# Kernel optimization log

Measured on AMD Instinct MI355X. Metric: run time of the kernel, lower is better.

The kernel has to match this reference:

```python
import jax, jax.numpy as jnp
import numpy as np

B, N, F, I = 4, 1024, 32, 8
DIM, DN, NF = 256, 64, 100
H, HD = 4, 64  # heads, head_dim (H*HD == DIM)
EPS = 1e-5


def setup_inputs() -> dict:
    key = jax.random.key(0)
    ks = jax.random.split(key, 24)
    def p(k, shape, s=0.05):
        return jax.random.normal(k, shape, jnp.float32) * s
    return {
        "x": jax.random.normal(ks[0], (B, N, F, I), jnp.float32),
        "idx": jax.random.randint(ks[1], (F,), 0, NF),
        "ctx": jax.random.normal(ks[2], (B, 1, DN), jnp.float32),
        "Wp": p(ks[3], (NF, DIM * I)),          # in_projection table
        "Bp": p(ks[4], (NF, DIM)),               # feature_bias table
        "q_emb": p(ks[5], (1, DIM)),             # queries table
        "cln_kv_W": p(ks[6], (DN, 2 * DIM)), "cln_kv_b": jnp.zeros((2 * DIM,), jnp.float32),
        "cln_q_W": p(ks[7], (DN, 2 * DIM)),  "cln_q_b": jnp.zeros((2 * DIM,), jnp.float32),
        "cln_h_W": p(ks[8], (DN, 2 * DIM)),  "cln_h_b": jnp.zeros((2 * DIM,), jnp.float32),
        "Wq": p(ks[9], (DIM, DIM)), "Wk": p(ks[10], (DIM, DIM)),
        "Wv": p(ks[11], (DIM, DIM)), "Wo": p(ks[12], (DIM, DIM)),
        "W1": p(ks[13], (DIM, 4 * DIM)), "b1": jnp.zeros((4 * DIM,), jnp.float32),
        "W2": p(ks[14], (4 * DIM, DIM)), "b2": jnp.zeros((DIM,), jnp.float32),
    }


def _ln(x):
    m = x.mean(-1, keepdims=True)
    v = ((x - m) ** 2).mean(-1, keepdims=True)
    return (x - m) * jax.lax.rsqrt(v + EPS)


def _cln(x, c, W, b):
    # adaptive layernorm: ln(x) * (1 + scale(ctx)) + shift(ctx)
    h = _ln(x)
    s, sh = jnp.split(c @ W + b, 2, axis=-1)
    return h * (1.0 + s) + sh


def reference(x, idx, ctx, Wp, Bp, q_emb, cln_kv_W, cln_kv_b, cln_q_W, cln_q_b,
              cln_h_W, cln_h_b, Wq, Wk, Wv, Wo, W1, b1, W2, b2):
    b_, n_, f_, i_ = x.shape
    # gather per-feature projection weights and biases
    w = Wp[idx].reshape(f_, DIM, i_)                 # [f, d, i]
    bias = Bp[idx][None]                              # [1, f, d] (broadcasts b,n)
    kv = jnp.einsum('bnfi,fdi->bnfd', x, w)           # [b, n, f, d]
    c = ctx[:, :, None, :]                            # [b, 1, 1, dn]
    kv = _cln(kv, c, cln_kv_W, cln_kv_b) + bias
    q = jnp.broadcast_to(q_emb[None, None], (b_, n_, 1, DIM))
    # cross-attention (pre-norm, conditional)
    qn = _cln(q, c, cln_q_W, cln_q_b)
    qh = (qn @ Wq).reshape(b_, n_, 1, H, HD)
    kh = (kv @ Wk).reshape(b_, n_, f_, H, HD)
    vh = (kv @ Wv).reshape(b_, n_, f_, H, HD)
    att = jnp.einsum('bnqhe,bnfhe->bnhqf', qh, kh) / np.sqrt(HD).astype(np.float32)
    att = jax.nn.softmax(att, axis=-1)
    o = jnp.einsum('bnhqf,bnfhe->bnqhe', att, vh).reshape(b_, n_, 1, DIM) @ Wo
    h = q + o
    # MLP (pre-norm, conditional)
    hn = _cln(h, c, cln_h_W, cln_h_b)
    h = h + (jax.nn.gelu(hn @ W1 + b1) @ W2 + b2)
    return h[:, :, 0, :]                              # squeeze query dim -> [b, n, d]
```

## Files before the change

kernel.cpp:

```cpp
#include <hip/hip_runtime.h>
#include <cmath>

#define EPSV 1e-5f
using f4 = float4;

typedef __attribute__((ext_vector_type(8))) short bfrag;
typedef __attribute__((ext_vector_type(4))) float ffrag;

#define WS_SKV   0
#define WS_SHKV  1024
#define WS_SH    2048
#define WS_SHH   3072
#define WS_A     4096
#define WS_R     8192
#define WS_HT    4202496
#define WS_L     5251072
#define WS_G     6299648
#define WS_GB    WS_G
#define WS_HNB   (WS_G + 2097152)
#define WS_W1T   (WS_G + 2621440)
#define WS_W2T   (WS_G + 2752512)
#define WS_MT    (WS_G + 2883584)

#define FMA8(acc, s, wa, wb) \
  acc[0]=fmaf((s),(wa).x,acc[0]); acc[1]=fmaf((s),(wa).y,acc[1]); \
  acc[2]=fmaf((s),(wa).z,acc[2]); acc[3]=fmaf((s),(wa).w,acc[3]); \
  acc[4]=fmaf((s),(wb).x,acc[4]); acc[5]=fmaf((s),(wb).y,acc[5]); \
  acc[6]=fmaf((s),(wb).z,acc[6]); acc[7]=fmaf((s),(wb).w,acc[7]);

#define DOT8(res, v, wa, wb) \
  res = fmaf((v)[0],(wa).x,res); res = fmaf((v)[1],(wa).y,res); \
  res = fmaf((v)[2],(wa).z,res); res = fmaf((v)[3],(wa).w,res); \
  res = fmaf((v)[4],(wb).x,res); res = fmaf((v)[5],(wb).y,res); \
  res = fmaf((v)[6],(wb).z,res); res = fmaf((v)[7],(wb).w,res);

__device__ __forceinline__ float bfly32(float v){
  v += __shfl_xor(v, 1);  v += __shfl_xor(v, 2);  v += __shfl_xor(v, 4);
  v += __shfl_xor(v, 8);  v += __shfl_xor(v, 16);
  return v;
}

template<int CTRL>
__device__ __forceinline__ float dpp_add(float v){
  int x = __builtin_bit_cast(int, v);
  int y = __builtin_amdgcn_update_dpp(0, x, CTRL, 0xf, 0xf, true);
  return v + __builtin_bit_cast(float, y);
}
__device__ __forceinline__ float red32(float v){
  v = dpp_add<0xB1>(v);
  v = dpp_add<0x4E>(v);
  v = dpp_add<0x124>(v);
  v = dpp_add<0x128>(v);
  v += __shfl_xor(v, 16);
  return v;
}

__device__ __forceinline__ float gelu_fast(float x){
  float z2 = 1.5957691216057308f*(x + 0.044715f*x*x*x);
  return x / (1.0f + __expf(-z2));
}

__device__ __forceinline__ unsigned short f2bf(float x){
  union { float f; unsigned u; } v; v.f = x;
  unsigned r = v.u + 0x7fffu + ((v.u >> 16) & 1u);
  return (unsigned short)(r >> 16);
}
__device__ __forceinline__ float bfu(unsigned short u){
  union { unsigned u; float f; } v; v.u = ((unsigned)u) << 16; return v.f;
}
__device__ __forceinline__ ushort4 comb4(ushort4 a, ushort4 b, float inv){
  ushort4 r;
  r.x = f2bf((bfu(a.x)+bfu(b.x))*inv);
  r.y = f2bf((bfu(a.y)+bfu(b.y))*inv);
  r.z = f2bf((bfu(a.z)+bfu(b.z))*inv);
  r.w = f2bf((bfu(a.w)+bfu(b.w))*inv);
  return r;
}

__global__ __launch_bounds__(256) void kwm_conv(
  const float* __restrict__ W1, const float* __restrict__ W2,
  const float* __restrict__ Wv, const float* __restrict__ Wo,
  float* __restrict__ ws)
{
  const int tid = threadIdx.x;
  int blk = blockIdx.x;
  if (blk < 128){
    __shared__ unsigned short lt[64][68];
    const float* src; unsigned short* dst; int K, N, K0, N0;
    if (blk < 64){
      src = W1; dst = (unsigned short*)(ws + WS_W1T);
      K = 256; N = 1024; K0 = (blk >> 4)*64; N0 = (blk & 15)*64;
    } else {
      blk -= 64;
      src = W2; dst = (unsigned short*)(ws + WS_W2T);
      K = 1024; N = 256; K0 = (blk >> 2)*64; N0 = (blk & 3)*64;
    }
    #pragma unroll
    for (int i=0;i<4;++i){
      int r = i*16 + (tid>>4);
      int c = (tid&15)*4;
      f4 v = *(const f4*)(src + (size_t)(K0+r)*N + N0 + c);
      lt[r][c]   = f2bf(v.x); lt[r][c+1] = f2bf(v.y);
      lt[r][c+2] = f2bf(v.z); lt[r][c+3] = f2bf(v.w);
    }
    __syncthreads();
    #pragma unroll
    for (int i=0;i<4;++i){
      int n  = i*16 + (tid>>4);
      int kc = (tid&15)*4;
      ushort4 u;
      u.x = lt[kc][n]; u.y = lt[kc+1][n]; u.z = lt[kc+2][n]; u.w = lt[kc+3][n];
      *(ushort4*)(dst + (size_t)(N0+n)*K + K0 + kc) = u;
    }
  } else {
    blk -= 128;
    __shared__ float wvs[4*64];
    __shared__ float wos[64*256];
    const int h   = blk >> 6;
    const int dg4 = blk & 63;
    {
      int d = tid >> 6, e = tid & 63;
      wvs[d*64+e] = Wv[(size_t)(dg4*4 + d)*256 + h*64 + e];
    }
    {
      int e = tid >> 2, c = (tid & 3)*64;
      const float* src = Wo + (size_t)(h*64 + e)*256 + c;
      #pragma unroll
      for (int i=0;i<16;++i)
        *(f4*)&wos[e*256 + c + i*4] = *(const f4*)(src + i*4);
    }
    __syncthreads();
    float acc[4] = {};
    for (int e=0;e<64;++e){
      float wo = wos[e*256 + tid];
      acc[0] = fmaf(wvs[0*64+e], wo, acc[0]);
      acc[1] = fmaf(wvs[1*64+e], wo, acc[1]);
      acc[2] = fmaf(wvs[2*64+e], wo, acc[2]);
      acc[3] = fmaf(wvs[3*64+e], wo, acc[3]);
    }
    unsigned short* Mt = (unsigned short*)(ws + WS_MT);
    ushort4 u;
    u.x = f2bf(acc[0]); u.y = f2bf(acc[1]); u.z = f2bf(acc[2]); u.w = f2bf(acc[3]);
    *(ushort4*)(Mt + (size_t)tid*1024 + h*256 + dg4*4) = u;
  }
}

__global__ __launch_bounds__(256) void k0_all(
    const float* __restrict__ ctx, const float* __restrict__ q_emb,
    const float* __restrict__ Wkv, const float* __restrict__ bkv,
    const float* __restrict__ Wqc, const float* __restrict__ bqc,
    const float* __restrict__ Whc, const float* __restrict__ bhc,
    const float* __restrict__ Wq,  const float* __restrict__ Wk,
    float* __restrict__ ws)
{
  const int b = blockIdx.x >> 2, h = blockIdx.x & 3;
  const int tid = threadIdx.x;
  __shared__ float c[64], qn[256], ph[256], qh64[64], red[8];
  if (tid < 64) c[tid] = ctx[b*64 + tid];
  __syncthreads();

  float skv = bkv[tid],      shkv = bkv[256+tid];
  float sq  = bqc[tid],      shq  = bqc[256+tid];
  float sh  = bhc[tid],      shh  = bhc[256+tid];
  #pragma unroll 8
  for (int j=0;j<64;++j){
    float cj = c[j];
    skv  = fmaf(cj, Wkv[j*512 + tid],       skv);
    shkv = fmaf(cj, Wkv[j*512 + 256 + tid], shkv);
    sq   = fmaf(cj, Wqc[j*512 + tid],       sq);
    shq  = fmaf(cj, Wqc[j*512 + 256 + tid], shq);
    sh   = fmaf(cj, Whc[j*512 + tid],       sh);
    shh  = fmaf(cj, Whc[j*512 + 256 + tid], shh);
  }
  if (h == 0){
    ws[WS_SKV  + b*256 + tid] = skv;
    ws[WS_SHKV + b*256 + tid] = shkv;
    ws[WS_SH   + b*256 + tid] = sh;
    ws[WS_SHH  + b*256 + tid] = shh;
  }

  float qe = q_emb[tid];
  float s1r = qe, s2r = qe*qe;
  for (int mm=1;mm<64;mm<<=1){ s1r += __shfl_xor(s1r,mm); s2r += __shfl_xor(s2r,mm); }
  int wv = tid>>6, ln = tid&63;
  if (ln==0){ red[wv*2]=s1r; red[wv*2+1]=s2r; }
  __syncthreads();
  float S1 = red[0]+red[2]+red[4]+red[6];
  float S2 = red[1]+red[3]+red[5]+red[7];
  float mean = S1*(1.0f/256.0f);
  float var  = S2*(1.0f/256.0f) - mean*mean;
  float rs   = rsqrtf(var + EPSV);
  qn[tid] = (qe-mean)*rs*(1.0f+sq) + shq;
  __syncthreads();

  {
    const int t = tid & 63, ks = tid >> 6;
    float p = 0.f;
    const float* wq = Wq + (size_t)(ks*64)*256 + h*64 + t;
    #pragma unroll 8
    for (int d=0; d<64; ++d) p = fmaf(qn[ks*64+d], wq[d*256], p);
    ph[tid] = p;
  }
  __syncthreads();
  if (tid < 64) qh64[tid] = ph[tid] + ph[64+tid] + ph[128+tid] + ph[192+tid];
  __syncthreads();

  {
    float a = 0.f;
    const float* wkr = Wk + (size_t)tid*256 + h*64;
    #pragma unroll
    for (int e4=0; e4<16; ++e4){
      f4 wv4 = *(const f4*)(wkr + e4*4);
      a = fmaf(qh64[e4*4+0], wv4.x, a);
      a = fmaf(qh64[e4*4+1], wv4.y, a);
      a = fmaf(qh64[e4*4+2], wv4.z, a);
      a = fmaf(qh64[e4*4+3], wv4.w, a);
    }
    ws[WS_A + b*1024 + h*256 + tid] = 0.125f*a;
  }
}

__global__ __launch_bounds__(256,4) void k1f_attn(
  const float* __restrict__ x, const int* __restrict__ idx,
  const float* __restrict__ Wp, const float* __restrict__ Bp,
  float* __restrict__ ws)
{
  __shared__ float xs[2048];
  __shared__ float wls[4096];

  const int tid = threadIdx.x;
  const int p0  = (blockIdx.x >> 1) * 8;
  const int half= blockIdx.x & 1;
  const int f0  = half * 16;
  const int b   = p0 >> 10;
  const int t   = tid >> 5;
  const int dg  = tid & 31;
  const int dA  = 4*dg, dB = 128 + 4*dg;

  {
    const float* xg = x + (size_t)p0*256 + tid*8;
    f4 a  = *(const f4*)xg;
    f4 bq = *(const f4*)(xg + 4);
    *(f4*)&xs[tid*8]     = a;
    *(f4*)&xs[tid*8 + 4] = bq;
  }
  f4 Ar[4][2];
  #pragma unroll
  for (int h=0;h<4;++h){
    Ar[h][0] = *(const f4*)(ws + WS_A + b*1024 + h*256 + dA);
    Ar[h][1] = *(const f4*)(ws + WS_A + b*1024 + h*256 + dB);
  }

  f4 skA = *(const f4*)(ws + WS_SKV  + b*256 + dA);
  f4 skB = *(const f4*)(ws + WS_SKV  + b*256 + dB);
  f4 shA = *(const f4*)(ws + WS_SHKV + b*256 + dA);
  f4 shB = *(const f4*)(ws + WS_SHKV + b*256 + dB);
  float coef[8] = {1.f+skA.x,1.f+skA.y,1.f+skA.z,1.f+skA.w,
                   1.f+skB.x,1.f+skB.y,1.f+skB.z,1.f+skB.w};
  float shk[8]  = {shA.x,shA.y,shA.z,shA.w, shB.x,shB.y,shB.z,shB.w};

  int r0 = idx[f0], r1 = idx[f0+1];
  f4 u0 = *(const f4*)(Wp + (size_t)r0*2048 + tid*8);
  f4 u1 = *(const f4*)(Wp + (size_t)r0*2048 + tid*8 + 4);
  f4 u2 = *(const f4*)(Wp + (size_t)r1*2048 + tid*8);
  f4 u3 = *(const f4*)(Wp + (size_t)r1*2048 + tid*8 + 4);

  float l[4] = {0.f,0.f,0.f,0.f};
  float racc[4][8] = {};

  for (int fi = 0; fi < 8; ++fi){
    const int f = f0 + fi*2;
    __syncthreads();
    wls[0*256+tid]=u0.x; wls[1*256+tid]=u0.y; wls[2*256+tid]=u0.z; wls[3*256+tid]=u0.w;
    wls[4*256+tid]=u1.x; wls[5*256+tid]=u1.y; wls[6*256+tid]=u1.z; wls[7*256+tid]=u1.w;
    wls[2048+0*256+tid]=u2.x; wls[2048+1*256+tid]=u2.y;
    wls[2048+2*256+tid]=u2.z; wls[2048+3*256+tid]=u2.w;
    wls[2048+4*256+tid]=u3.x; wls[2048+5*256+tid]=u3.y;
    wls[2048+6*256+tid]=u3.z; wls[2048+7*256+tid]=u3.w;
    __syncthreads();

    f4 ba0 = *(const f4*)(Bp + (size_t)r0*256 + dA);
    f4 bb0 = *(const f4*)(Bp + (size_t)r0*256 + dB);
    f4 ba1 = *(const f4*)(Bp + (size_t)r1*256 + dA);
    f4 bb1 = *(const f4*)(Bp + (size_t)r1*256 + dB);

    const int fn = (fi < 7) ? f + 2 : f0;
    int rn0 = idx[fn], rn1 = idx[fn+1];
    u0 = *(const f4*)(Wp + (size_t)rn0*2048 + tid*8);
    u1 = *(const f4*)(Wp + (size_t)rn0*2048 + tid*8 + 4);
    u2 = *(const f4*)(Wp + (size_t)rn1*2048 + tid*8);
    u3 = *(const f4*)(Wp + (size_t)rn1*2048 + tid*8 + 4);

    #pragma unroll
    for (int sub=0; sub<2; ++sub){
      const float* wrow = wls + sub*2048;
      const int fc = f + sub;
      f4 ba = sub ? ba1 : ba0;
      f4 bb = sub ? bb1 : bb0;

      f4 xa = *(const f4*)&xs[t*256 + fc*8];
      f4 xb = *(const f4*)&xs[t*256 + fc*8 + 4];
      float xf[8] = {xa.x,xa.y,xa.z,xa.w, xb.x,xb.y,xb.z,xb.w};

      float val[8] = {};
      #pragma unroll
      for (int i=0;i<8;++i){
        f4 wa  = *(const f4*)&wrow[i*256 + dA];
        f4 wbv = *(const f4*)&wrow[i*256 + dB];
        FMA8(val, xf[i], wa, wbv);
      }

      float s=0.f, ss=0.f;
      #pragma unroll
      for (int jj=0;jj<8;++jj){ s += val[jj]; ss = fmaf(val[jj],val[jj],ss); }
      s = red32(s); ss = red32(ss);
      float mean = s*(1.f/256.f);
      float var  = ss*(1.f/256.f) - mean*mean;
      float rsg  = rsqrtf(var + EPSV);
      float mrs  = mean*rsg;

      float off[8] = {shk[0]+ba.x, shk[1]+ba.y, shk[2]+ba.z, shk[3]+ba.w,
                      shk[4]+bb.x, shk[5]+bb.y, shk[6]+bb.z, shk[7]+bb.w};
      float kvl[8];
      #pragma unroll
      for (int jj=0;jj<8;++jj)
        kvl[jj] = fmaf(fmaf(val[jj], rsg, -mrs), coef[jj], off[jj]);

      #pragma unroll
      for (int h=0;h<4;++h){
        float lg = 0.f;
        DOT8(lg, kvl, Ar[h][0], Ar[h][1]);
        lg = red32(lg);
        float pp = __expf(lg);
        l[h] += pp;
        #pragma unroll
        for (int jj=0;jj<8;++jj)
          racc[h][jj] = fmaf(pp, kvl[jj], racc[h][jj]);
      }
    }
    r0 = rn0; r1 = rn1;
  }

  unsigned short* Pr = (unsigned short*)(ws + WS_R);
  size_t base = (size_t)(half*4096 + p0 + t) * 1024;
  #pragma unroll
  for (int h=0;h<4;++h){
    ushort4 ua, ub;
    ua.x=f2bf(racc[h][0]); ua.y=f2bf(racc[h][1]); ua.z=f2bf(racc[h][2]); ua.w=f2bf(racc[h][3]);
    ub.x=f2bf(racc[h][4]); ub.y=f2bf(racc[h][5]); ub.z=f2bf(racc[h][6]); ub.w=f2bf(racc[h][7]);
    *(ushort4*)(Pr + base + h*256 + dA) = ua;
    *(ushort4*)(Pr + base + h*256 + dB) = ub;
  }
  if (dg == 0){
    float* Lp = ws + WS_L;
    #pragma unroll
    for (int h=0;h<4;++h) Lp[(size_t)(half*4096 + p0 + t)*4 + h] = l[h];
  }
}

__global__ __launch_bounds__(256) void k2g_mfma(float* __restrict__ ws)
{
  __shared__ unsigned short aT[2][32*40];
  __shared__ unsigned short bT[2][64*40];
  __shared__ float invs[128];
  const unsigned short* P0 = (const unsigned short*)(ws + WS_R);
  const unsigned short* P1 = P0 + 4194304;
  const unsigned short* mt = (const unsigned short*)(ws + WS_MT);
  const float* Lp = ws + WS_L;

  const int tid = threadIdx.x;
  const int M0 = (blockIdx.x >> 2) * 32;
  const int N0 = (blockIdx.x & 3) * 64;
  const int lane = tid & 63;
  const int wid = tid >> 6;
  const int wm = wid >> 1, wn = wid & 1;
  const int m16 = lane & 15, q = lane >> 4;

  const int sa_m = tid >> 3, sa_k = (tid & 7) * 4;
  const int sb_n = tid >> 2, sb_k = (tid & 3) * 8;

  if (tid < 128){
    int lt = tid >> 2, h = tid & 3;
    invs[tid] = 1.f / (Lp[(size_t)(M0 + lt)*4 + h] +
                       Lp[(size_t)(4096 + M0 + lt)*4 + h]);
  }

  ushort4 ua0 = *(const ushort4*)(P0 + (size_t)(M0 + sa_m)*1024 + sa_k);
  ushort4 ua1 = *(const ushort4*)(P1 + (size_t)(M0 + sa_m)*1024 + sa_k);
  f4 ub = *(const f4*)(mt + (size_t)(N0 + sb_n)*1024 + sb_k);
  __syncthreads();

  ffrag acc[2];
  acc[0] = (ffrag){0.f,0.f,0.f,0.f};
  acc[1] = (ffrag){0.f,0.f,0.f,0.f};

  for (int ks=0; ks<32; ++ks){
    const int buf = ks & 1;
    float inv = invs[sa_m*4 + (ks >> 3)];
    *(ushort4*)&aT[buf][sa_m*40 + sa_k] = comb4(ua0, ua1, inv);
    *(f4*)&bT[buf][sb_n*40 + sb_k]      = ub;
    __syncthreads();
    int kn = (ks < 31) ? ks+1 : 31;
    ua0 = *(const ushort4*)(P0 + (size_t)(M0 + sa_m)*1024 + kn*32 + sa_k);
    ua1 = *(const ushort4*)(P1 + (size_t)(M0 + sa_m)*1024 + kn*32 + sa_k);
    ub  = *(const f4*)(mt + (size_t)(N0 + sb_n)*1024 + kn*32 + sb_k);

    bfrag af, bf0, bf1;
    af  = *(const bfrag*)&aT[buf][(wm*16 + m16)*40 + q*8];
    bf0 = *(const bfrag*)&bT[buf][(wn*32 + m16)*40 + q*8];
    bf1 = *(const bfrag*)&bT[buf][(wn*32 + 16 + m16)*40 + q*8];
    acc[0] = __builtin_amdgcn_mfma_f32_16x16x32_bf16(bf0, af, acc[0], 0, 0, 0);
    acc[1] = __builtin_amdgcn_mfma_f32_16x16x32_bf16(bf1, af, acc[1], 0, 0, 0);
  }

  const int m = M0 + wm*16 + m16;
  #pragma unroll
  for (int j=0;j<2;++j){
    const int n4 = N0 + wn*32 + j*16 + q*4;
    *(f4*)(ws + WS_HT + (size_t)m*256 + n4) =
      make_float4(acc[j][0], acc[j][1], acc[j][2], acc[j][3]);
  }
}

__global__ __launch_bounds__(256) void ke_ln(
  const float* __restrict__ q_emb, float* __restrict__ ws)
{
  const int tid = threadIdx.x;
  const int p0 = blockIdx.x * 8;
  const int b  = p0 >> 10;
  const int tq = tid >> 5, jq = tid & 31;
  const int cA = 4*jq, cB = 128 + 4*jq;

  float* op = ws + WS_HT + (size_t)(p0+tq)*256;
  f4 oA = *(const f4*)(op + cA);
  f4 oB = *(const f4*)(op + cB);
  f4 qA = *(const f4*)(q_emb + cA);
  f4 qB = *(const f4*)(q_emb + cB);
  float ht[8] = {oA.x+qA.x, oA.y+qA.y, oA.z+qA.z, oA.w+qA.w,
                 oB.x+qB.x, oB.y+qB.y, oB.z+qB.z, oB.w+qB.w};
  float s=0.f, ss=0.f;
  #pragma unroll
  for (int jj=0;jj<8;++jj){ s += ht[jj]; ss = fmaf(ht[jj],ht[jj],ss); }
  s = bfly32(s); ss = bfly32(ss);
  float mean = s*(1.f/256.f);
  float var  = ss*(1.f/256.f) - mean*mean;
  float rsg  = rsqrtf(var + EPSV);
  f4 sH0 = *(const f4*)(ws + WS_SH  + b*256 + cA);
  f4 sH1 = *(const f4*)(ws + WS_SH  + b*256 + cB);
  f4 hH0 = *(const f4*)(ws + WS_SHH + b*256 + cA);
  f4 hH1 = *(const f4*)(ws + WS_SHH + b*256 + cB);
  float sHv[8]  = {sH0.x,sH0.y,sH0.z,sH0.w, sH1.x,sH1.y,sH1.z,sH1.w};
  float hHv[8]  = {hH0.x,hH0.y,hH0.z,hH0.w, hH1.x,hH1.y,hH1.z,hH1.w};
  float hnv[8];
  #pragma unroll
  for (int jj=0;jj<8;++jj)
    hnv[jj] = (ht[jj]-mean)*rsg*(1.f+sHv[jj]) + hHv[jj];

  *(f4*)(op+cA) = make_float4(ht[0],ht[1],ht[2],ht[3]);
  *(f4*)(op+cB) = make_float4(ht[4],ht[5],ht[6],ht[7]);
  unsigned short* hnb = (unsigned short*)(ws + WS_HNB);
  ushort4 uA, uB;
  uA.x=f2bf(hnv[0]); uA.y=f2bf(hnv[1]); uA.z=f2bf(hnv[2]); uA.w=f2bf(hnv[3]);
  uB.x=f2bf(hnv[4]); uB.y=f2bf(hnv[5]); uB.z=f2bf(hnv[6]); uB.w=f2bf(hnv[7]);
  *(ushort4*)(hnb + (size_t)(p0+tq)*256 + cA) = uA;
  *(ushort4*)(hnb + (size_t)(p0+tq)*256 + cB) = uB;
}

__global__ __launch_bounds__(256) void k3_mfma(
  const float* __restrict__ b1, float* __restrict__ ws)
{
  __shared__ unsigned short aT[2][64*40];
  __shared__ unsigned short bT[2][128*40];
  const unsigned short* hnb = (const unsigned short*)(ws + WS_HNB);
  const unsigned short* w1t = (const unsigned short*)(ws + WS_W1T);
  unsigned short* gb = (unsigned short*)(ws + WS_GB);

  const int tid = threadIdx.x;
  const int M0 = (blockIdx.x >> 3) * 64;
  const int N0 = (blockIdx.x & 7) * 128;
  const int lane = tid & 63;
  const int wid = tid >> 6;
  const int wm = wid >> 1, wn = wid & 1;
  const int m16 = lane & 15, q = lane >> 4;

  const int sa_m = tid >> 2, sa_k = (tid & 3) * 8;
  const int sb_n = tid >> 1, sb_k = (tid & 1) * 16;

  f4 ua, ub0, ub1;
  ua  = *(const f4*)(hnb + (size_t)(M0 + sa_m)*256 + sa_k);
  ub0 = *(const f4*)(w1t + (size_t)(N0 + sb_n)*256 + sb_k);
  ub1 = *(const f4*)(w1t + (size_t)(N0 + sb_n)*256 + sb_k + 8);

  ffrag acc[2][4];
  #pragma unroll
  for (int i=0;i<2;++i)
    #pragma unroll
    for (int j=0;j<4;++j) acc[i][j] = (ffrag){0.f,0.f,0.f,0.f};

  for (int ks=0; ks<8; ++ks){
    const int buf = ks & 1;
    *(f4*)&aT[buf][sa_m*40 + sa_k]     = ua;
    *(f4*)&bT[buf][sb_n*40 + sb_k]     = ub0;
    *(f4*)&bT[buf][sb_n*40 + sb_k + 8] = ub1;
    __syncthreads();
    int kn = (ks < 7) ? ks+1 : 7;
    ua  = *(const f4*)(hnb + (size_t)(M0 + sa_m)*256 + kn*32 + sa_k);
    ub0 = *(const f4*)(w1t + (size_t)(N0 + sb_n)*256 + kn*32 + sb_k);
    ub1 = *(const f4*)(w1t + (size_t)(N0 + sb_n)*256 + kn*32 + sb_k + 8);

    bfrag af[2], bf_[4];
    af[0] = *(const bfrag*)&aT[buf][(wm*32 + m16)*40 + q*8];
    af[1] = *(const bfrag*)&aT[buf][(wm*32 + 16 + m16)*40 + q*8];
    #pragma unroll
    for (int j=0;j<4;++j)
      bf_[j] = *(const bfrag*)&bT[buf][(wn*64 + j*16 + m16)*40 + q*8];
    #pragma unroll
    for (int i=0;i<2;++i)
      #pragma unroll
      for (int j=0;j<4;++j)
        acc[i][j] = __builtin_amdgcn_mfma_f32_16x16x32_bf16(bf_[j], af[i], acc[i][j], 0, 0, 0);
  }

  #pragma unroll
  for (int i=0;i<2;++i){
    const int m = M0 + wm*32 + i*16 + m16;
    #pragma unroll
    for (int j=0;j<4;++j){
      const int n4 = N0 + wn*64 + j*16 + q*4;
      f4 bv = *(const f4*)(b1 + n4);
      ushort4 u;
      u.x = f2bf(gelu_fast(acc[i][j][0] + bv.x));
      u.y = f2bf(gelu_fast(acc[i][j][1] + bv.y));
      u.z = f2bf(gelu_fast(acc[i][j][2] + bv.z));
      u.w = f2bf(gelu_fast(acc[i][j][3] + bv.w));
      *(ushort4*)(gb + (size_t)m*1024 + n4) = u;
    }
  }
}

__global__ __launch_bounds__(256) void k4_mfma(
  const float* __restrict__ b2, const float* __restrict__ ws_c,
  float* __restrict__ ws, float* __restrict__ out)
{
  __shared__ unsigned short aT[2][32*40];
  __shared__ unsigned short bT[2][64*40];
  const unsigned short* gb  = (const unsigned short*)(ws_c + WS_GB);
  const unsigned short* w2t = (const unsigned short*)(ws_c + WS_W2T);

  const int tid = threadIdx.x;
  const int M0 = (blockIdx.x >> 2) * 32;
  const int N0 = (blockIdx.x & 3) * 64;
  const int lane = tid & 63;
  const int wid = tid >> 6;
  const int wm = wid >> 1, wn = wid & 1;
  const int m16 = lane & 15, q = lane >> 4;

  const int sa_m = tid >> 3, sa_k = (tid & 7) * 4;
  const int sb_n = tid >> 2, sb_k = (tid & 3) * 8;

  ushort4 ua;
  f4 ub;
  ua = *(const ushort4*)(gb  + (size_t)(M0 + sa_m)*1024 + sa_k);
  ub = *(const f4*)(w2t + (size_t)(N0 + sb_n)*1024 + sb_k);

  ffrag acc[2];
  acc[0] = (ffrag){0.f,0.f,0.f,0.f};
  acc[1] = (ffrag){0.f,0.f,0.f,0.f};

  for (int ks=0; ks<32; ++ks){
    const int buf = ks & 1;
    *(ushort4*)&aT[buf][sa_m*40 + sa_k] = ua;
    *(f4*)&bT[buf][sb_n*40 + sb_k]      = ub;
    __syncthreads();
    int kn = (ks < 31) ? ks+1 : 31;
    ua = *(const ushort4*)(gb  + (size_t)(M0 + sa_m)*1024 + kn*32 + sa_k);
    ub = *(const f4*)(w2t + (size_t)(N0 + sb_n)*1024 + kn*32 + sb_k);

    bfrag af, bf0, bf1;
    af  = *(const bfrag*)&aT[buf][(wm*16 + m16)*40 + q*8];
    bf0 = *(const bfrag*)&bT[buf][(wn*32 + m16)*40 + q*8];
    bf1 = *(const bfrag*)&bT[buf][(wn*32 + 16 + m16)*40 + q*8];
    acc[0] = __builtin_amdgcn_mfma_f32_16x16x32_bf16(bf0, af, acc[0], 0, 0, 0);
    acc[1] = __builtin_amdgcn_mfma_f32_16x16x32_bf16(bf1, af, acc[1], 0, 0, 0);
  }

  const int m = M0 + wm*16 + m16;
  #pragma unroll
  for (int j=0;j<2;++j){
    const int n4 = N0 + wn*32 + j*16 + q*4;
    f4 bv = *(const f4*)(b2 + n4);
    f4 hv = *(const f4*)(ws + WS_HT + (size_t)m*256 + n4);
    *(f4*)(out + (size_t)m*256 + n4) =
      make_float4(acc[j][0]+bv.x+hv.x, acc[j][1]+bv.y+hv.y,
                  acc[j][2]+bv.z+hv.z, acc[j][3]+bv.w+hv.w);
  }
}

extern "C" void kernel_launch(void* const* d_in, const int* in_sizes, int n_in,
                              void* d_out, int out_size, void* d_ws, size_t ws_size,
                              hipStream_t stream)
{
  const float* x    = (const float*)d_in[0];
  const int*   idx  = (const int*)  d_in[1];
  const float* ctx  = (const float*)d_in[2];
  const float* Wp   = (const float*)d_in[3];
  const float* Bp   = (const float*)d_in[4];
  const float* qemb = (const float*)d_in[5];
  const float* Wkv  = (const float*)d_in[6];
  const float* bkv  = (const float*)d_in[7];
  const float* Wqc  = (const float*)d_in[8];
  const float* bqc  = (const float*)d_in[9];
  const float* Whc  = (const float*)d_in[10];
  const float* bhc  = (const float*)d_in[11];
  const float* Wq   = (const float*)d_in[12];
  const float* Wk   = (const float*)d_in[13];
  const float* Wv   = (const float*)d_in[14];
  const float* Wo   = (const float*)d_in[15];
  const float* W1   = (const float*)d_in[16];
  const float* b1   = (const float*)d_in[17];
  const float* W2   = (const float*)d_in[18];
  const float* b2   = (const float*)d_in[19];
  float* ws  = (float*)d_ws;
  float* out = (float*)d_out;

  hipLaunchKernelGGL(kwm_conv, dim3(384),  dim3(256), 0, stream, W1, W2, Wv, Wo, ws);
  hipLaunchKernelGGL(k0_all,   dim3(16),   dim3(256), 0, stream,
                     ctx, qemb, Wkv, bkv, Wqc, bqc, Whc, bhc, Wq, Wk, ws);
  hipLaunchKernelGGL(k1f_attn, dim3(1024), dim3(256), 0, stream, x, idx, Wp, Bp, ws);
  hipLaunchKernelGGL(k2g_mfma, dim3(512),  dim3(256), 0, stream, ws);
  hipLaunchKernelGGL(ke_ln,    dim3(512),  dim3(256), 0, stream, qemb, ws);
  hipLaunchKernelGGL(k3_mfma,  dim3(512),  dim3(256), 0, stream, b1, ws);
  hipLaunchKernelGGL(k4_mfma,  dim3(512),  dim3(256), 0, stream, b2, ws, ws, out);
}
```

Before: 193.8 us.

## Merge prep kernels, process two tokens per attention thread, fuse output GEMM with LN

```diff
diff --git a/kernel.cpp b/kernel.cpp
--- a/kernel.cpp
+++ b/kernel.cpp
@@ -77,15 +77,25 @@
   return r;
 }
 
-__global__ __launch_bounds__(256) void kwm_conv(
+__global__ __launch_bounds__(256) void kprep(
   const float* __restrict__ W1, const float* __restrict__ W2,
   const float* __restrict__ Wv, const float* __restrict__ Wo,
+  const float* __restrict__ ctx, const float* __restrict__ q_emb,
+  const float* __restrict__ Wkv, const float* __restrict__ bkv,
+  const float* __restrict__ Wqc, const float* __restrict__ bqc,
+  const float* __restrict__ Whc, const float* __restrict__ bhc,
+  const float* __restrict__ Wq,  const float* __restrict__ Wk,
   float* __restrict__ ws)
 {
   const int tid = threadIdx.x;
   int blk = blockIdx.x;
+  __shared__ union {
+    unsigned short lt[64][68];
+    struct { float wvs[4*64]; float wos[64*256]; } m;
+    struct { float c[64], qn[256], ph[256], qh64[64], red[8]; } z;
+  } sm;
+
   if (blk < 128){
-    __shared__ unsigned short lt[64][68];
     const float* src; unsigned short* dst; int K, N, K0, N0;
     if (blk < 64){
       src = W1; dst = (unsigned short*)(ws + WS_W1T);
@@ -100,8 +110,8 @@
       int r = i*16 + (tid>>4);
       int c = (tid&15)*4;
       f4 v = *(const f4*)(src + (size_t)(K0+r)*N + N0 + c);
-      lt[r][c]   = f2bf(v.x); lt[r][c+1] = f2bf(v.y);
-      lt[r][c+2] = f2bf(v.z); lt[r][c+3] = f2bf(v.w);
+      sm.lt[r][c]   = f2bf(v.x); sm.lt[r][c+1] = f2bf(v.y);
+      sm.lt[r][c+2] = f2bf(v.z); sm.lt[r][c+3] = f2bf(v.w);
     }
     __syncthreads();
     #pragma unroll
@@ -109,127 +119,115 @@
       int n  = i*16 + (tid>>4);
       int kc = (tid&15)*4;
       ushort4 u;
-      u.x = lt[kc][n]; u.y = lt[kc+1][n]; u.z = lt[kc+2][n]; u.w = lt[kc+3][n];
+      u.x = sm.lt[kc][n]; u.y = sm.lt[kc+1][n]; u.z = sm.lt[kc+2][n]; u.w = sm.lt[kc+3][n];
       *(ushort4*)(dst + (size_t)(N0+n)*K + K0 + kc) = u;
     }
-  } else {
+  } else if (blk < 384){
     blk -= 128;
-    __shared__ float wvs[4*64];
-    __shared__ float wos[64*256];
     const int h   = blk >> 6;
     const int dg4 = blk & 63;
     {
       int d = tid >> 6, e = tid & 63;
-      wvs[d*64+e] = Wv[(size_t)(dg4*4 + d)*256 + h*64 + e];
+      sm.m.wvs[d*64+e] = Wv[(size_t)(dg4*4 + d)*256 + h*64 + e];
     }
     {
       int e = tid >> 2, c = (tid & 3)*64;
       const float* src = Wo + (size_t)(h*64 + e)*256 + c;
       #pragma unroll
       for (int i=0;i<16;++i)
-        *(f4*)&wos[e*256 + c + i*4] = *(const f4*)(src + i*4);
+        *(f4*)&sm.m.wos[e*256 + c + i*4] = *(const f4*)(src + i*4);
     }
     __syncthreads();
     float acc[4] = {};
     for (int e=0;e<64;++e){
-      float wo = wos[e*256 + tid];
-      acc[0] = fmaf(wvs[0*64+e], wo, acc[0]);
-      acc[1] = fmaf(wvs[1*64+e], wo, acc[1]);
-      acc[2] = fmaf(wvs[2*64+e], wo, acc[2]);
-      acc[3] = fmaf(wvs[3*64+e], wo, acc[3]);
+      float wo = sm.m.wos[e*256 + tid];
+      acc[0] = fmaf(sm.m.wvs[0*64+e], wo, acc[0]);
+      acc[1] = fmaf(sm.m.wvs[1*64+e], wo, acc[1]);
+      acc[2] = fmaf(sm.m.wvs[2*64+e], wo, acc[2]);
+      acc[3] = fmaf(sm.m.wvs[3*64+e], wo, acc[3]);
     }
     unsigned short* Mt = (unsigned short*)(ws + WS_MT);
     ushort4 u;
     u.x = f2bf(acc[0]); u.y = f2bf(acc[1]); u.z = f2bf(acc[2]); u.w = f2bf(acc[3]);
     *(ushort4*)(Mt + (size_t)tid*1024 + h*256 + dg4*4) = u;
-  }
-}
-
-__global__ __launch_bounds__(256) void k0_all(
-    const float* __restrict__ ctx, const float* __restrict__ q_emb,
-    const float* __restrict__ Wkv, const float* __restrict__ bkv,
-    const float* __restrict__ Wqc, const float* __restrict__ bqc,
-    const float* __restrict__ Whc, const float* __restrict__ bhc,
-    const float* __restrict__ Wq,  const float* __restrict__ Wk,
-    float* __restrict__ ws)
-{
-  const int b = blockIdx.x >> 2, h = blockIdx.x & 3;
-  const int tid = threadIdx.x;
-  __shared__ float c[64], qn[256], ph[256], qh64[64], red[8];
-  if (tid < 64) c[tid] = ctx[b*64 + tid];
-  __syncthreads();
-
-  float skv = bkv[tid],      shkv = bkv[256+tid];
-  float sq  = bqc[tid],      shq  = bqc[256+tid];
-  float sh  = bhc[tid],      shh  = bhc[256+tid];
-  #pragma unroll 8
-  for (int j=0;j<64;++j){
-    float cj = c[j];
-    skv  = fmaf(cj, Wkv[j*512 + tid],       skv);
-    shkv = fmaf(cj, Wkv[j*512 + 256 + tid], shkv);
-    sq   = fmaf(cj, Wqc[j*512 + tid],       sq);
-    shq  = fmaf(cj, Wqc[j*512 + 256 + tid], shq);
-    sh   = fmaf(cj, Whc[j*512 + tid],       sh);
-    shh  = fmaf(cj, Whc[j*512 + 256 + tid], shh);
-  }
-  if (h == 0){
-    ws[WS_SKV  + b*256 + tid] = skv;
-    ws[WS_SHKV + b*256 + tid] = shkv;
-    ws[WS_SH   + b*256 + tid] = sh;
-    ws[WS_SHH  + b*256 + tid] = shh;
-  }
-
-  float qe = q_emb[tid];
-  float s1r = qe, s2r = qe*qe;
-  for (int mm=1;mm<64;mm<<=1){ s1r += __shfl_xor(s1r,mm); s2r += __shfl_xor(s2r,mm); }
-  int wv = tid>>6, ln = tid&63;
-  if (ln==0){ red[wv*2]=s1r; red[wv*2+1]=s2r; }
-  __syncthreads();
-  float S1 = red[0]+red[2]+red[4]+red[6];
-  float S2 = red[1]+red[3]+red[5]+red[7];
-  float mean = S1*(1.0f/256.0f);
-  float var  = S2*(1.0f/256.0f) - mean*mean;
-  float rs   = rsqrtf(var + EPSV);
-  qn[tid] = (qe-mean)*rs*(1.0f+sq) + shq;
-  __syncthreads();
-
-  {
-    const int t = tid & 63, ks = tid >> 6;
-    float p = 0.f;
-    const float* wq = Wq + (size_t)(ks*64)*256 + h*64 + t;
+  } else {
+    blk -= 384;
+    const int b = blk >> 2, h = blk & 3;
+    if (tid < 64) sm.z.c[tid] = ctx[b*64 + tid];
+    __syncthreads();
+
+    float skv = bkv[tid],      shkv = bkv[256+tid];
+    float sq  = bqc[tid],      shq  = bqc[256+tid];
+    float sh  = bhc[tid],      shh  = bhc[256+tid];
     #pragma unroll 8
-    for (int d=0; d<64; ++d) p = fmaf(qn[ks*64+d], wq[d*256], p);
-    ph[tid] = p;
-  }
-  __syncthreads();
-  if (tid < 64) qh64[tid] = ph[tid] + ph[64+tid] + ph[128+tid] + ph[192+tid];
-  __syncthreads();
-
-  {
-    float a = 0.f;
-    const float* wkr = Wk + (size_t)tid*256 + h*64;
-    #pragma unroll
-    for (int e4=0; e4<16; ++e4){
-      f4 wv4 = *(const f4*)(wkr + e4*4);
-      a = fmaf(qh64[e4*4+0], wv4.x, a);
-      a = fmaf(qh64[e4*4+1], wv4.y, a);
-      a = fmaf(qh64[e4*4+2], wv4.z, a);
-      a = fmaf(qh64[e4*4+3], wv4.w, a);
-    }
-    ws[WS_A + b*1024 + h*256 + tid] = 0.125f*a;
-  }
-}
-
-__global__ __launch_bounds__(256,4) void k1f_attn(
+    for (int j=0;j<64;++j){
+      float cj = sm.z.c[j];
+      skv  = fmaf(cj, Wkv[j*512 + tid],       skv);
+      shkv = fmaf(cj, Wkv[j*512 + 256 + tid], shkv);
+      sq   = fmaf(cj, Wqc[j*512 + tid],       sq);
+      shq  = fmaf(cj, Wqc[j*512 + 256 + tid], shq);
+      sh   = fmaf(cj, Whc[j*512 + tid],       sh);
+      shh  = fmaf(cj, Whc[j*512 + 256 + tid], shh);
+    }
+    if (h == 0){
+      ws[WS_SKV  + b*256 + tid] = skv;
+      ws[WS_SHKV + b*256 + tid] = shkv;
+      ws[WS_SH   + b*256 + tid] = sh;
+      ws[WS_SHH  + b*256 + tid] = shh;
+    }
+
+    float qe = q_emb[tid];
+    float s1r = qe, s2r = qe*qe;
+    for (int mm=1;mm<64;mm<<=1){ s1r += __shfl_xor(s1r,mm); s2r += __shfl_xor(s2r,mm); }
+    int wv = tid>>6, ln = tid&63;
+    if (ln==0){ sm.z.red[wv*2]=s1r; sm.z.red[wv*2+1]=s2r; }
+    __syncthreads();
+    float S1 = sm.z.red[0]+sm.z.red[2]+sm.z.red[4]+sm.z.red[6];
+    float S2 = sm.z.red[1]+sm.z.red[3]+sm.z.red[5]+sm.z.red[7];
+    float mean = S1*(1.0f/256.0f);
+    float var  = S2*(1.0f/256.0f) - mean*mean;
+    float rs   = rsqrtf(var + EPSV);
+    sm.z.qn[tid] = (qe-mean)*rs*(1.0f+sq) + shq;
+    __syncthreads();
+
+    {
+      const int t = tid & 63, ks = tid >> 6;
+      float p = 0.f;
+      const float* wq = Wq + (size_t)(ks*64)*256 + h*64 + t;
+      #pragma unroll 8
+      for (int d=0; d<64; ++d) p = fmaf(sm.z.qn[ks*64+d], wq[d*256], p);
+      sm.z.ph[tid] = p;
+    }
+    __syncthreads();
+    if (tid < 64) sm.z.qh64[tid] = sm.z.ph[tid] + sm.z.ph[64+tid] + sm.z.ph[128+tid] + sm.z.ph[192+tid];
+    __syncthreads();
+
+    {
+      float a = 0.f;
+      const float* wkr = Wk + (size_t)tid*256 + h*64;
+      #pragma unroll
+      for (int e4=0; e4<16; ++e4){
+        f4 wv4 = *(const f4*)(wkr + e4*4);
+        a = fmaf(sm.z.qh64[e4*4+0], wv4.x, a);
+        a = fmaf(sm.z.qh64[e4*4+1], wv4.y, a);
+        a = fmaf(sm.z.qh64[e4*4+2], wv4.z, a);
+        a = fmaf(sm.z.qh64[e4*4+3], wv4.w, a);
+      }
+      ws[WS_A + b*1024 + h*256 + tid] = 0.125f*a;
+    }
+  }
+}
+
+__global__ __launch_bounds__(256,2) void k1f_attn(
   const float* __restrict__ x, const int* __restrict__ idx,
   const float* __restrict__ Wp, const float* __restrict__ Bp,
   float* __restrict__ ws)
 {
-  __shared__ float xs[2048];
+  __shared__ float xs[4096];
   __shared__ float wls[4096];
 
   const int tid = threadIdx.x;
-  const int p0  = (blockIdx.x >> 1) * 8;
+  const int p0  = (blockIdx.x >> 1) * 16;
   const int half= blockIdx.x & 1;
   const int f0  = half * 16;
   const int b   = p0 >> 10;
@@ -243,6 +241,10 @@
     f4 bq = *(const f4*)(xg + 4);
     *(f4*)&xs[tid*8]     = a;
     *(f4*)&xs[tid*8 + 4] = bq;
+    f4 a2  = *(const f4*)(xg + 2048);
+    f4 bq2 = *(const f4*)(xg + 2048 + 4);
+    *(f4*)&xs[2048 + tid*8]     = a2;
+    *(f4*)&xs[2048 + tid*8 + 4] = bq2;
   }
   f4 Ar[4][2];
   #pragma unroll
@@ -265,8 +267,8 @@
   f4 u2 = *(const f4*)(Wp + (size_t)r1*2048 + tid*8);
   f4 u3 = *(const f4*)(Wp + (size_t)r1*2048 + tid*8 + 4);
 
-  float l[4] = {0.f,0.f,0.f,0.f};
-  float racc[4][8] = {};
+  float l[2][4] = {};
+  float racc[2][4][8] = {};
 
   for (int fi = 0; fi < 8; ++fi){
     const int f = f0 + fi*2;
@@ -298,172 +300,195 @@
       f4 ba = sub ? ba1 : ba0;
       f4 bb = sub ? bb1 : bb0;
 
-      f4 xa = *(const f4*)&xs[t*256 + fc*8];
-      f4 xb = *(const f4*)&xs[t*256 + fc*8 + 4];
-      float xf[8] = {xa.x,xa.y,xa.z,xa.w, xb.x,xb.y,xb.z,xb.w};
-
-      float val[8] = {};
+      float xf0[8], xf1[8];
+      {
+        f4 xa = *(const f4*)&xs[t*256 + fc*8];
+        f4 xb = *(const f4*)&xs[t*256 + fc*8 + 4];
+        xf0[0]=xa.x; xf0[1]=xa.y; xf0[2]=xa.z; xf0[3]=xa.w;
+        xf0[4]=xb.x; xf0[5]=xb.y; xf0[6]=xb.z; xf0[7]=xb.w;
+        f4 xc = *(const f4*)&xs[(t+8)*256 + fc*8];
+        f4 xd = *(const f4*)&xs[(t+8)*256 + fc*8 + 4];
+        xf1[0]=xc.x; xf1[1]=xc.y; xf1[2]=xc.z; xf1[3]=xc.w;
+        xf1[4]=xd.x; xf1[5]=xd.y; xf1[6]=xd.z; xf1[7]=xd.w;
+      }
+
+      float val[2][8] = {};
       #pragma unroll
       for (int i=0;i<8;++i){
         f4 wa  = *(const f4*)&wrow[i*256 + dA];
         f4 wbv = *(const f4*)&wrow[i*256 + dB];
-        FMA8(val, xf[i], wa, wbv);
+        FMA8(val[0], xf0[i], wa, wbv);
+        FMA8(val[1], xf1[i], wa, wbv);
       }
-
-      float s=0.f, ss=0.f;
-      #pragma unroll
-      for (int jj=0;jj<8;++jj){ s += val[jj]; ss = fmaf(val[jj],val[jj],ss); }
-      s = red32(s); ss = red32(ss);
-      float mean = s*(1.f/256.f);
-      float var  = ss*(1.f/256.f) - mean*mean;
-      float rsg  = rsqrtf(var + EPSV);
-      float mrs  = mean*rsg;
 
       float off[8] = {shk[0]+ba.x, shk[1]+ba.y, shk[2]+ba.z, shk[3]+ba.w,
                       shk[4]+bb.x, shk[5]+bb.y, shk[6]+bb.z, shk[7]+bb.w};
-      float kvl[8];
+
       #pragma unroll
-      for (int jj=0;jj<8;++jj)
-        kvl[jj] = fmaf(fmaf(val[jj], rsg, -mrs), coef[jj], off[jj]);
-
-      #pragma unroll
-      for (int h=0;h<4;++h){
-        float lg = 0.f;
-        DOT8(lg, kvl, Ar[h][0], Ar[h][1]);
-        lg = red32(lg);
-        float pp = __expf(lg);
-        l[h] += pp;
+      for (int tt=0; tt<2; ++tt){
+        float s=0.f, ss=0.f;
+        #pragma unroll
+        for (int jj=0;jj<8;++jj){ s += val[tt][jj]; ss = fmaf(val[tt][jj],val[tt][jj],ss); }
+        s = red32(s); ss = red32(ss);
+        float mean = s*(1.f/256.f);
+        float var  = ss*(1.f/256.f) - mean*mean;
+        float rsg  = rsqrtf(var + EPSV);
+        float mrs  = mean*rsg;
+
+        float kvl[8];
         #pragma unroll
         for (int jj=0;jj<8;++jj)
-          racc[h][jj] = fmaf(pp, kvl[jj], racc[h][jj]);
+          kvl[jj] = fmaf(fmaf(val[tt][jj], rsg, -mrs), coef[jj], off[jj]);
+
+        #pragma unroll
+        for (int h=0;h<4;++h){
+          float lg = 0.f;
+          DOT8(lg, kvl, Ar[h][0], Ar[h][1]);
+          lg = red32(lg);
+          float pp = __expf(lg);
+          l[tt][h] += pp;
+          #pragma unroll
+          for (int jj=0;jj<8;++jj)
+            racc[tt][h][jj] = fmaf(pp, kvl[jj], racc[tt][h][jj]);
+        }
       }
     }
     r0 = rn0; r1 = rn1;
   }
 
   unsigned short* Pr = (unsigned short*)(ws + WS_R);
-  size_t base = (size_t)(half*4096 + p0 + t) * 1024;
-  #pragma unroll
-  for (int h=0;h<4;++h){
-    ushort4 ua, ub;
-    ua.x=f2bf(racc[h][0]); ua.y=f2bf(racc[h][1]); ua.z=f2bf(racc[h][2]); ua.w=f2bf(racc[h][3]);
-    ub.x=f2bf(racc[h][4]); ub.y=f2bf(racc[h][5]); ub.z=f2bf(racc[h][6]); ub.w=f2bf(racc[h][7]);
-    *(ushort4*)(Pr + base + h*256 + dA) = ua;
-    *(ushort4*)(Pr + base + h*256 + dB) = ub;
+  #pragma unroll
+  for (int tt=0; tt<2; ++tt){
+    size_t base = (size_t)(half*4096 + p0 + t + tt*8) * 1024;
+    #pragma unroll
+    for (int h=0;h<4;++h){
+      ushort4 ua, ub;
+      ua.x=f2bf(racc[tt][h][0]); ua.y=f2bf(racc[tt][h][1]);
+      ua.z=f2bf(racc[tt][h][2]); ua.w=f2bf(racc[tt][h][3]);
+      ub.x=f2bf(racc[tt][h][4]); ub.y=f2bf(racc[tt][h][5]);
+      ub.z=f2bf(racc[tt][h][6]); ub.w=f2bf(racc[tt][h][7]);
+      *(ushort4*)(Pr + base + h*256 + dA) = ua;
+      *(ushort4*)(Pr + base + h*256 + dB) = ub;
+    }
   }
   if (dg == 0){
     float* Lp = ws + WS_L;
     #pragma unroll
-    for (int h=0;h<4;++h) Lp[(size_t)(half*4096 + p0 + t)*4 + h] = l[h];
-  }
-}
-
-__global__ __launch_bounds__(256) void k2g_mfma(float* __restrict__ ws)
+    for (int tt=0; tt<2; ++tt)
+      #pragma unroll
+      for (int h=0;h<4;++h)
+        Lp[(size_t)(half*4096 + p0 + t + tt*8)*4 + h] = l[tt][h];
+  }
+}
+
+__global__ __launch_bounds__(256) void k2e_mfma(
+  const float* __restrict__ q_emb, float* __restrict__ ws)
 {
-  __shared__ unsigned short aT[2][32*40];
-  __shared__ unsigned short bT[2][64*40];
-  __shared__ float invs[128];
+  __shared__ unsigned short aT[2][16*40];
+  __shared__ unsigned short bT[2][256*40];
+  __shared__ float invs[64];
+  __shared__ float red[128];
   const unsigned short* P0 = (const unsigned short*)(ws + WS_R);
   const unsigned short* P1 = P0 + 4194304;
   const unsigned short* mt = (const unsigned short*)(ws + WS_MT);
   const float* Lp = ws + WS_L;
 
   const int tid = threadIdx.x;
-  const int M0 = (blockIdx.x >> 2) * 32;
-  const int N0 = (blockIdx.x & 3) * 64;
+  const int M0  = blockIdx.x * 16;
+  const int b   = M0 >> 10;
   const int lane = tid & 63;
-  const int wid = tid >> 6;
-  const int wm = wid >> 1, wn = wid & 1;
-  const int m16 = lane & 15, q = lane >> 4;
+  const int wid  = tid >> 6;
+  const int m16  = lane & 15, q = lane >> 4;
 
   const int sa_m = tid >> 3, sa_k = (tid & 7) * 4;
-  const int sb_n = tid >> 2, sb_k = (tid & 3) * 8;
-
-  if (tid < 128){
+  if (tid < 64){
     int lt = tid >> 2, h = tid & 3;
     invs[tid] = 1.f / (Lp[(size_t)(M0 + lt)*4 + h] +
                        Lp[(size_t)(4096 + M0 + lt)*4 + h]);
   }
 
-  ushort4 ua0 = *(const ushort4*)(P0 + (size_t)(M0 + sa_m)*1024 + sa_k);
-  ushort4 ua1 = *(const ushort4*)(P1 + (size_t)(M0 + sa_m)*1024 + sa_k);
-  f4 ub = *(const f4*)(mt + (size_t)(N0 + sb_n)*1024 + sb_k);
+  ushort4 ua0, ua1;
+  if (tid < 128){
+    ua0 = *(const ushort4*)(P0 + (size_t)(M0 + sa_m)*1024 + sa_k);
+    ua1 = *(const ushort4*)(P1 + (size_t)(M0 + sa_m)*1024 + sa_k);
+  }
+  f4 ub[4];
+  #pragma unroll
+  for (int i=0;i<4;++i)
+    ub[i] = *(const f4*)(mt + (size_t)tid*1024 + i*8);
   __syncthreads();
 
-  ffrag acc[2];
-  acc[0] = (ffrag){0.f,0.f,0.f,0.f};
-  acc[1] = (ffrag){0.f,0.f,0.f,0.f};
+  ffrag acc[4];
+  #pragma unroll
+  for (int j=0;j<4;++j) acc[j] = (ffrag){0.f,0.f,0.f,0.f};
 
   for (int ks=0; ks<32; ++ks){
     const int buf = ks & 1;
-    float inv = invs[sa_m*4 + (ks >> 3)];
-    *(ushort4*)&aT[buf][sa_m*40 + sa_k] = comb4(ua0, ua1, inv);
-    *(f4*)&bT[buf][sb_n*40 + sb_k]      = ub;
+    if (tid < 128){
+      float inv = invs[sa_m*4 + (ks >> 3)];
+      *(ushort4*)&aT[buf][sa_m*40 + sa_k] = comb4(ua0, ua1, inv);
+    }
+    #pragma unroll
+    for (int i=0;i<4;++i)
+      *(f4*)&bT[buf][tid*40 + i*8] = ub[i];
     __syncthreads();
     int kn = (ks < 31) ? ks+1 : 31;
-    ua0 = *(const ushort4*)(P0 + (size_t)(M0 + sa_m)*1024 + kn*32 + sa_k);
-    ua1 = *(const ushort4*)(P1 + (size_t)(M0 + sa_m)*1024 + kn*32 + sa_k);
-    ub  = *(const f4*)(mt + (size_t)(N0 + sb_n)*1024 + kn*32 + sb_k);
-
-    bfrag af, bf0, bf1;
-    af  = *(const bfrag*)&aT[buf][(wm*16 + m16)*40 + q*8];
-    bf0 = *(const bfrag*)&bT[buf][(wn*32 + m16)*40 + q*8];
-    bf1 = *(const bfrag*)&bT[buf][(wn*32 + 16 + m16)*40 + q*8];
-    acc[0] = __builtin_amdgcn_mfma_f32_16x16x32_bf16(bf0, af, acc[0], 0, 0, 0);
-    acc[1] = __builtin_amdgcn_mfma_f32_16x16x32_bf16(bf1, af, acc[1], 0, 0, 0);
-  }
-
-  const int m = M0 + wm*16 + m16;
-  #pragma unroll
-  for (int j=0;j<2;++j){
-    const int n4 = N0 + wn*32 + j*16 + q*4;
+    if (tid < 128){
+      ua0 = *(const ushort4*)(P0 + (size_t)(M0 + sa_m)*1024 + kn*32 + sa_k);
+      ua1 = *(const ushort4*)(P1 + (size_t)(M0 + sa_m)*1024 + kn*32 + sa_k);
+    }
+    #pragma unroll
+    for (int i=0;i<4;++i)
+      ub[i] = *(const f4*)(mt + (size_t)tid*1024 + kn*32 + i*8);
+
+    bfrag af = *(const bfrag*)&aT[buf][m16*40 + q*8];
+    #pragma unroll
+    for (int j=0;j<4;++j){
+      bfrag bf = *(const bfrag*)&bT[buf][(wid*64 + j*16 + m16)*40 + q*8];
+      acc[j] = __builtin_amdgcn_mfma_f32_16x16x32_bf16(bf, af, acc[j], 0, 0, 0);
+    }
+  }
+
+  float htv[4][4];
+  float s = 0.f, ss = 0.f;
+  #pragma unroll
+  for (int j=0;j<4;++j){
+    const int n4 = wid*64 + j*16 + q*4;
+    f4 qe = *(const f4*)(q_emb + n4);
+    htv[j][0] = acc[j][0] + qe.x;
+    htv[j][1] = acc[j][1] + qe.y;
+    htv[j][2] = acc[j][2] + qe.z;
+    htv[j][3] = acc[j][3] + qe.w;
+    #pragma unroll
+    for (int r=0;r<4;++r){ s += htv[j][r]; ss = fmaf(htv[j][r], htv[j][r], ss); }
+  }
+  s  += __shfl_xor(s, 16);  s  += __shfl_xor(s, 32);
+  ss += __shfl_xor(ss, 16); ss += __shfl_xor(ss, 32);
+  if (q == 0){ red[wid*32 + m16*2] = s; red[wid*32 + m16*2 + 1] = ss; }
+  __syncthreads();
+  float S  = red[m16*2]     + red[32 + m16*2]     + red[64 + m16*2]     + red[96 + m16*2];
+  float SS = red[m16*2 + 1] + red[32 + m16*2 + 1] + red[64 + m16*2 + 1] + red[96 + m16*2 + 1];
+  float mean = S*(1.f/256.f);
+  float var  = SS*(1.f/256.f) - mean*mean;
+  float rsg  = rsqrtf(var + EPSV);
+
+  unsigned short* hnb = (unsigned short*)(ws + WS_HNB);
+  const int m = M0 + m16;
+  #pragma unroll
+  for (int j=0;j<4;++j){
+    const int n4 = wid*64 + j*16 + q*4;
+    f4 sH = *(const f4*)(ws + WS_SH  + b*256 + n4);
+    f4 hH = *(const f4*)(ws + WS_SHH + b*256 + n4);
+    float hn0 = (htv[j][0]-mean)*rsg*(1.f+sH.x) + hH.x;
+    float hn1 = (htv[j][1]-mean)*rsg*(1.f+sH.y) + hH.y;
+    float hn2 = (htv[j][2]-mean)*rsg*(1.f+sH.z) + hH.z;
+    float hn3 = (htv[j][3]-mean)*rsg*(1.f+sH.w) + hH.w;
     *(f4*)(ws + WS_HT + (size_t)m*256 + n4) =
-      make_float4(acc[j][0], acc[j][1], acc[j][2], acc[j][3]);
-  }
-}
-
-__global__ __launch_bounds__(256) void ke_ln(
-  const float* __restrict__ q_emb, float* __restrict__ ws)
-{
-  const int tid = threadIdx.x;
-  const int p0 = blockIdx.x * 8;
-  const int b  = p0 >> 10;
-  const int tq = tid >> 5, jq = tid & 31;
-  const int cA = 4*jq, cB = 128 + 4*jq;
-
-  float* op = ws + WS_HT + (size_t)(p0+tq)*256;
-  f4 oA = *(const f4*)(op + cA);
-  f4 oB = *(const f4*)(op + cB);
-  f4 qA = *(const f4*)(q_emb + cA);
-  f4 qB = *(const f4*)(q_emb + cB);
-  float ht[8] = {oA.x+qA.x, oA.y+qA.y, oA.z+qA.z, oA.w+qA.w,
-                 oB.x+qB.x, oB.y+qB.y, oB.z+qB.z, oB.w+qB.w};
-  float s=0.f, ss=0.f;
-  #pragma unroll
-  for (int jj=0;jj<8;++jj){ s += ht[jj]; ss = fmaf(ht[jj],ht[jj],ss); }
-  s = bfly32(s); ss = bfly32(ss);
-  float mean = s*(1.f/256.f);
-  float var  = ss*(1.f/256.f) - mean*mean;
-  float rsg  = rsqrtf(var + EPSV);
-  f4 sH0 = *(const f4*)(ws + WS_SH  + b*256 + cA);
-  f4 sH1 = *(const f4*)(ws + WS_SH  + b*256 + cB);
-  f4 hH0 = *(const f4*)(ws + WS_SHH + b*256 + cA);
-  f4 hH1 = *(const f4*)(ws + WS_SHH + b*256 + cB);
-  float sHv[8]  = {sH0.x,sH0.y,sH0.z,sH0.w, sH1.x,sH1.y,sH1.z,sH1.w};
-  float hHv[8]  = {hH0.x,hH0.y,hH0.z,hH0.w, hH1.x,hH1.y,hH1.z,hH1.w};
-  float hnv[8];
-  #pragma unroll
-  for (int jj=0;jj<8;++jj)
-    hnv[jj] = (ht[jj]-mean)*rsg*(1.f+sHv[jj]) + hHv[jj];
-
-  *(f4*)(op+cA) = make_float4(ht[0],ht[1],ht[2],ht[3]);
-  *(f4*)(op+cB) = make_float4(ht[4],ht[5],ht[6],ht[7]);
-  unsigned short* hnb = (unsigned short*)(ws + WS_HNB);
-  ushort4 uA, uB;
-  uA.x=f2bf(hnv[0]); uA.y=f2bf(hnv[1]); uA.z=f2bf(hnv[2]); uA.w=f2bf(hnv[3]);
-  uB.x=f2bf(hnv[4]); uB.y=f2bf(hnv[5]); uB.z=f2bf(hnv[6]); uB.w=f2bf(hnv[7]);
-  *(ushort4*)(hnb + (size_t)(p0+tq)*256 + cA) = uA;
-  *(ushort4*)(hnb + (size_t)(p0+tq)*256 + cB) = uB;
+      make_float4(htv[j][0], htv[j][1], htv[j][2], htv[j][3]);
+    ushort4 u;
+    u.x = f2bf(hn0); u.y = f2bf(hn1); u.z = f2bf(hn2); u.w = f2bf(hn3);
+    *(ushort4*)(hnb + (size_t)m*256 + n4) = u;
+  }
 }
 
 __global__ __launch_bounds__(256) void k3_mfma(
@@ -623,12 +648,10 @@
   float* ws  = (float*)d_ws;
   float* out = (float*)d_out;
 
-  hipLaunchKernelGGL(kwm_conv, dim3(384),  dim3(256), 0, stream, W1, W2, Wv, Wo, ws);
-  hipLaunchKernelGGL(k0_all,   dim3(16),   dim3(256), 0, stream,
-                     ctx, qemb, Wkv, bkv, Wqc, bqc, Whc, bhc, Wq, Wk, ws);
-  hipLaunchKernelGGL(k1f_attn, dim3(1024), dim3(256), 0, stream, x, idx, Wp, Bp, ws);
-  hipLaunchKernelGGL(k2g_mfma, dim3(512),  dim3(256), 0, stream, ws);
-  hipLaunchKernelGGL(ke_ln,    dim3(512),  dim3(256), 0, stream, qemb, ws);
+  hipLaunchKernelGGL(kprep,    dim3(400),  dim3(256), 0, stream,
+                     W1, W2, Wv, Wo, ctx, qemb, Wkv, bkv, Wqc, bqc, Whc, bhc, Wq, Wk, ws);
+  hipLaunchKernelGGL(k1f_attn, dim3(512),  dim3(256), 0, stream, x, idx, Wp, Bp, ws);
+  hipLaunchKernelGGL(k2e_mfma, dim3(256),  dim3(256), 0, stream, qemb, ws);
   hipLaunchKernelGGL(k3_mfma,  dim3(512),  dim3(256), 0, stream, b1, ws);
   hipLaunchKernelGGL(k4_mfma,  dim3(512),  dim3(256), 0, stream, b2, ws, ws, out);
 }
```

New measurement: 216.8 us. 11.8% more time.
